# Kernel tuning notes

Measured on AMD Instinct MI355X. Metric: run time of the kernel, lower is better.

Reference implementation:

```python
import jax, jax.numpy as jnp
import numpy as np

B, N, DIM = 4, 2048, 3
H = 128          # hidden
K = 32           # num_neighbours
L = 4            # num_layers
OUT = 6          # out_per_particle


def _dense_init(key, fan_in, fan_out):
    kw, kb = jax.random.split(key)
    w = jax.random.normal(kw, (fan_in, fan_out), jnp.float32) / np.sqrt(fan_in)
    b = jnp.zeros((fan_out,), jnp.float32)
    return w, b


def setup_inputs() -> dict:
    key = jax.random.key(0)
    ks = jax.random.split(key, 8)
    x = jax.random.normal(ks[0], (B, N, DIM), jnp.float32)
    embed_w, embed_b = _dense_init(ks[1], DIM, H)
    # per-layer stacked params
    miw, mib, mow, mob, uiw, uib, uow, uob = [], [], [], [], [], [], [], []
    for l in range(L):
        k0, k1, k2, k3 = jax.random.split(jax.random.fold_in(ks[2], l), 4)
        w, b = _dense_init(k0, 2 * H + 1, H); miw.append(w); mib.append(b)
        w, b = _dense_init(k1, H, H);         mow.append(w); mob.append(b)
        w, b = _dense_init(k2, 2 * H, H);     uiw.append(w); uib.append(b)
        w, b = _dense_init(k3, H, H);         uow.append(w); uob.append(b)
    out_w, out_b = _dense_init(ks[3], H, OUT)
    return {
        'x': x,
        'embed_w': embed_w, 'embed_b': embed_b,
        'msg_in_w': jnp.stack(miw), 'msg_in_b': jnp.stack(mib),
        'msg_out_w': jnp.stack(mow), 'msg_out_b': jnp.stack(mob),
        'upd_in_w': jnp.stack(uiw), 'upd_in_b': jnp.stack(uib),
        'upd_out_w': jnp.stack(uow), 'upd_out_b': jnp.stack(uob),
        'out_w': out_w, 'out_b': out_b,
    }


def reference(x, embed_w, embed_b,
              msg_in_w, msg_in_b, msg_out_w, msg_out_b,
              upd_in_w, upd_in_b, upd_out_w, upd_out_b,
              out_w, out_b):
    act = jax.nn.silu
    n = x.shape[-2]
    # per-particle embed: (B,N,H)
    h = x @ embed_w + embed_b
    # pairwise squared distances (B,N,N), plain Euclidean (geometry=None)
    diff = x[..., :, None, :] - x[..., None, :, :]
    d_sq = jnp.sum(diff * diff, axis=-1)
    eye = jnp.eye(n, dtype=bool)
    d_sq = jnp.where(eye, jnp.inf, d_sq)
    neg_topk, idx_topk = jax.lax.top_k(-d_sq, K)      # (B,N,K)
    d_nearest = jnp.sqrt(jnp.maximum(-neg_topk, 0.0))  # (B,N,K)

    gather = jax.vmap(lambda hb, ib: hb[ib])  # (N,H),(N,K)->(N,K,H) over batch
    n_layers = msg_in_w.shape[0]
    for l in range(n_layers):
        nb = gather(h, idx_topk)                               # (B,N,K,H)
        node_i = jnp.broadcast_to(h[..., :, None, :], nb.shape)
        msg_inp = jnp.concatenate([node_i, nb, d_nearest[..., None]], axis=-1)
        msg = act(msg_inp @ msg_in_w[l] + msg_in_b[l]) @ msg_out_w[l] + msg_out_b[l]
        agg = jnp.sum(msg, axis=-2)                            # (B,N,H)
        upd_inp = jnp.concatenate([h, agg], axis=-1)
        upd = act(upd_inp @ upd_in_w[l] + upd_in_b[l]) @ upd_out_w[l] + upd_out_b[l]
        h = h + upd
    return h @ out_w + out_b
```

## Files before the change

### kernel.cpp

```cpp
#include <hip/hip_runtime.h>
#include <math.h>

#define B_ 4
#define N_ 2048
#define H_ 128
#define K_ 32
#define L_ 4
#define OUT_ 6
#define BN_ (B_*N_)
#define NPB_L 16
#define LBLK 512

typedef __attribute__((ext_vector_type(8))) short short8;
typedef __attribute__((ext_vector_type(4))) float f32x4;

#define LDW (H_ + 8)
#define LAYER_W 98304
#define OFF_W1A 0
#define OFF_W1C 16384
#define OFF_W2  32768
#define OFF_U1  49152
#define OFF_U2  81920
#define SCAP 256
#define KNN_ROWS 4
#define KNN_BLKS (BN_/KNN_ROWS)
#define PREP_BLKS (L_*LAYER_W/256)

__device__ __forceinline__ float silu_f(float x) {
    return __fdividef(x, 1.0f + __expf(-x));
}
__device__ __forceinline__ short f2b(float f) {
    unsigned u = __float_as_uint(f);
    return (short)((u + 0x7FFFu + ((u >> 16) & 1u)) >> 16);
}
__device__ __forceinline__ float b2f(short s) {
    return __uint_as_float(((unsigned)(unsigned short)s) << 16);
}
__device__ __forceinline__ unsigned pack2(short lo, short hi) {
    return (unsigned)(unsigned short)lo | ((unsigned)(unsigned short)hi << 16);
}
__device__ __forceinline__ int mbcnt64(unsigned long long m) {
    return __builtin_amdgcn_mbcnt_hi((unsigned)(m >> 32),
           __builtin_amdgcn_mbcnt_lo((unsigned)m, 0));
}

__global__ __launch_bounds__(256) void k_front(
    const float* __restrict__ x, int* __restrict__ nidx, float* __restrict__ ndist,
    const float* __restrict__ miw, const float* __restrict__ mow,
    const float* __restrict__ uiw, const float* __restrict__ uow,
    short* __restrict__ wt,
    const float* __restrict__ ew, const float* __restrict__ eb,
    const float* __restrict__ mib, float* __restrict__ Epack)
{
    __shared__ float xsx[N_], xsy[N_], xsz[N_];
    __shared__ unsigned skey[KNN_ROWS][SCAP];
    __shared__ int      sid [KNN_ROWS][SCAP];

    if (blockIdx.x >= KNN_BLKS + PREP_BLKS) {
        int t = threadIdx.x;
        int which = t >> 7, n = t & 127;
        const float* W = miw + (size_t)(which ? 128 : 0) * H_;
        float E0 = 0.f, E1 = 0.f, E2 = 0.f, Eb = 0.f;
        for (int k = 0; k < 128; ++k) {
            float w = W[(size_t)k*H_ + n];
            E0 = fmaf(ew[k],       w, E0);
            E1 = fmaf(ew[128 + k], w, E1);
            E2 = fmaf(ew[256 + k], w, E2);
            Eb = fmaf(eb[k],       w, Eb);
        }
        float* dst = Epack + which * 512;
        dst[0*128 + n] = E0;
        dst[1*128 + n] = E1;
        dst[2*128 + n] = E2;
        dst[3*128 + n] = Eb + (which ? 0.f : mib[n]);
        return;
    }
    if (blockIdx.x >= KNN_BLKS) {
        int gid = (blockIdx.x - KNN_BLKS) * 256 + threadIdx.x;
        int l = gid / LAYER_W, o = gid - l * LAYER_W;
        float v;
        if (o < OFF_W1C) {
            int n = o >> 7, k = o & 127;
            v = miw[(size_t)l*257*H_ + k*H_ + n];
        } else if (o < OFF_W2) {
            int oo = o - OFF_W1C, n = oo >> 7, k = oo & 127;
            v = miw[(size_t)l*257*H_ + (128 + k)*H_ + n];
        } else if (o < OFF_U1) {
            int oo = o - OFF_W2, n = oo >> 7, k = oo & 127;
            v = mow[(size_t)l*H_*H_ + k*H_ + n];
        } else if (o < OFF_U2) {
            int oo = o - OFF_U1, n = oo >> 8, k = oo & 255;
            v = uiw[(size_t)l*2*H_*H_ + k*H_ + n];
        } else {
            int oo = o - OFF_U2, n = oo >> 7, k = oo & 127;
            v = uow[(size_t)l*H_*H_ + k*H_ + n];
        }
        wt[gid] = f2b(v);
        return;
    }

    int b  = blockIdx.x / (N_/KNN_ROWS);
    int i0 = (blockIdx.x % (N_/KNN_ROWS)) * KNN_ROWS;
    const float* xb = x + (size_t)b*N_*3;
    for (int t = threadIdx.x; t < N_*3; t += 256) {
        float v = xb[t];
        int q = t / 3, r = t - q*3;
        float* dst = (r == 0) ? xsx : (r == 1) ? xsy : xsz;
        dst[q] = v;
    }
    __syncthreads();

    int wave = threadIdx.x >> 6, lane = threadIdx.x & 63;
    int i = i0 + wave;
    float xix = xsx[i], xiy = xsy[i], xiz = xsz[i];

    unsigned u[N_/64];
    unsigned lmin = 0xFFFFFFFFu;
#pragma unroll
    for (int t = 0; t < N_/64; ++t) {
        int j = lane + 64*t;
        float d0 = xix-xsx[j], d1 = xiy-xsy[j], d2 = xiz-xsz[j];
        float d = d0*d0 + d1*d1 + d2*d2;
        unsigned k = (j == i) ? 0x7F800000u : __float_as_uint(d);
        u[t] = k;
        lmin = min(lmin, k);
    }
    unsigned mn = lmin, mx = lmin;
    for (int off = 32; off; off >>= 1) {
        unsigned o1 = (unsigned)__shfl_xor((int)mn, off); mn = min(mn, o1);
        unsigned o2 = (unsigned)__shfl_xor((int)mx, off); mx = max(mx, o2);
    }
    unsigned Tup = mn;
    if (mn != mx) {
        int hb = 31 - __clz((int)(mn ^ mx));
        Tup = mn & ~((2u << hb) - 1u);
        for (int bit = hb; bit >= 0; --bit) {
            unsigned cand = Tup | (1u << bit);
            if (__popcll(__ballot(lmin < cand)) < K_) Tup = cand;
        }
    }
    unsigned* sk = skey[wave];
    int*      si = sid [wave];
    int base = 0;
#pragma unroll
    for (int t = 0; t < N_/64; ++t) {
        bool pr = (u[t] <= Tup);
        unsigned long long m = __ballot(pr);
        if (pr) {
            int pos = base + mbcnt64(m);
            if (pos < SCAP) { sk[pos] = u[t]; si[pos] = lane + 64*t; }
        }
        base += __popcll(m);
    }
    int c = min(base, SCAP);
    unsigned sv[4]; int iv[4];
#pragma unroll
    for (int q = 0; q < 4; ++q) {
        int slot = lane + 64*q;
        bool ok = slot < c;
        sv[q] = ok ? sk[slot] : 0xFFFFFFFFu;
        iv[q] = ok ? si[slot] : 0;
    }
    unsigned T = mn;
    if (mn != Tup) {
        int hb = 31 - __clz((int)(mn ^ Tup));
        T = mn & ~((2u << hb) - 1u);
        for (int bit = hb; bit >= 0; --bit) {
            unsigned cand = T | (1u << bit);
            int cnt = __popcll(__ballot(sv[0] < cand)) + __popcll(__ballot(sv[1] < cand))
                    + __popcll(__ballot(sv[2] < cand)) + __popcll(__ballot(sv[3] < cand));
            if (cnt < K_) T = cand;
        }
    }
    int cnt_lt = __popcll(__ballot(sv[0] < T)) + __popcll(__ballot(sv[1] < T))
               + __popcll(__ballot(sv[2] < T)) + __popcll(__ballot(sv[3] < T));
    int need = K_ - cnt_lt;
    size_t rbase = ((size_t)(b*N_ + i)) * K_;
    int ltc = 0, eqc = 0;
#pragma unroll
    for (int q = 0; q < 4; ++q) {
        bool lt = sv[q] < T, eq = sv[q] == T;
        unsigned long long mlt = __ballot(lt), meq = __ballot(eq);
        int pp = ltc + mbcnt64(mlt), ee = eqc + mbcnt64(meq);
        ltc += __popcll(mlt); eqc += __popcll(meq);
        int pos = lt ? pp : ((eq && ee < need) ? (cnt_lt + ee) : -1);
        if (pos >= 0) {
            nidx [rbase + pos] = iv[q];
            ndist[rbase + pos] = sqrtf(__uint_as_float(sv[q]));
        }
    }
}

__global__ __launch_bounds__(LBLK, 4) void k_layer0(
    float* __restrict__ h, short* __restrict__ a,
    const int* __restrict__ nidx, const float* __restrict__ ndist,
    const float* __restrict__ wd,
    const short* __restrict__ wl,
    const float* __restrict__ b2, const float* __restrict__ u1b,
    const float* __restrict__ u2b,
    short* __restrict__ c_wr,
    const short* __restrict__ wn, const float* __restrict__ b1n,
    const float* __restrict__ x, const float* __restrict__ ew,
    const float* __restrict__ eb, const float* __restrict__ Epack)
{
    __shared__ __align__(16) short s_l[NPB_L][LDW];
    __shared__ __align__(16) short h_l[NPB_L][LDW];
    __shared__ __align__(16) short agg_l[NPB_L][LDW];
    __shared__ __align__(16) float h32s[NPB_L][H_];
    __shared__ float xjs[NPB_L][K_][3];
    __shared__ float dst_s[NPB_L][K_];
    int blk = blockIdx.x;
    int batch = (blk & 7) >> 1;
    int sub   = ((blk >> 3) << 1) | (blk & 1);
    int node0 = batch * N_ + sub * NPB_L;
    int tid = threadIdx.x;
    int wave = tid >> 6, lane = tid & 63, l15 = lane & 15, quad = lane >> 4;
    int ncol = wave*16 + l15;

    for (int t = tid; t < NPB_L*H_; t += LBLK) {
        int row = t >> 7, ch = t & 127;
        int gr = node0 + row;
        float v = eb[ch];
        v = fmaf(x[gr*3+0], ew[ch], v);
        v = fmaf(x[gr*3+1], ew[H_+ch], v);
        v = fmaf(x[gr*3+2], ew[2*H_+ch], v);
        h_l[row][ch] = f2b(v);
        h32s[row][ch] = v;
    }
    {
        int j = nidx[(size_t)node0*K_ + tid];
        int sm = tid >> 5, sk = tid & 31;
        dst_s[sm][sk] = ndist[(size_t)node0*K_ + tid];
        const float* xp = x + ((size_t)batch*N_ + j)*3;
        xjs[sm][sk][0] = xp[0]; xjs[sm][sk][1] = xp[1]; xjs[sm][sk][2] = xp[2];
    }
    __syncthreads();

    short8 bw2[4], bu1[8], bu2[4];
#pragma unroll
    for (int kk = 0; kk < 4; ++kk)
        bw2[kk] = *(const short8*)(wl + OFF_W2 + (size_t)ncol*H_ + kk*32 + quad*8);
#pragma unroll
    for (int kk = 0; kk < 8; ++kk)
        bu1[kk] = *(const short8*)(wl + OFF_U1 + (size_t)ncol*2*H_ + kk*32 + quad*8);
#pragma unroll
    for (int kk = 0; kk < 4; ++kk)
        bu2[kk] = *(const short8*)(wl + OFF_U2 + (size_t)ncol*H_ + kk*32 + quad*8);

    {
        float wd0 = wd[2*lane], wd1 = wd[2*lane+1];
        int ch0 = 2*lane, ch1 = 2*lane + 1;
        float Ea00 = Epack[ch0],       Ea01 = Epack[ch1];
        float Ea10 = Epack[128+ch0],   Ea11 = Epack[128+ch1];
        float Ea20 = Epack[256+ch0],   Ea21 = Epack[256+ch1];
        float ea0  = Epack[384+ch0],   ea1  = Epack[384+ch1];
        float Ec00 = Epack[512+ch0],   Ec01 = Epack[512+ch1];
        float Ec10 = Epack[640+ch0],   Ec11 = Epack[640+ch1];
        float Ec20 = Epack[768+ch0],   Ec21 = Epack[768+ch1];
        float ec0  = Epack[896+ch0],   ec1  = Epack[896+ch1];
#pragma unroll
        for (int nn = 0; nn < 2; ++nn) {
            int m = wave*2 + nn;
            int gr = node0 + m;
            float xi0 = x[gr*3], xi1 = x[gr*3+1], xi2 = x[gr*3+2];
            float a0 = fmaf(xi2, Ea20, fmaf(xi1, Ea10, fmaf(xi0, Ea00, ea0)));
            float a1 = fmaf(xi2, Ea21, fmaf(xi1, Ea11, fmaf(xi0, Ea01, ea1)));
            float s0 = 0.f, s1 = 0.f;
#pragma unroll
            for (int k = 0; k < K_; ++k) {
                float xj0 = xjs[m][k][0], xj1 = xjs[m][k][1], xj2 = xjs[m][k][2];
                float dd = dst_s[m][k];
                float c0 = fmaf(xj2, Ec20, fmaf(xj1, Ec10, fmaf(xj0, Ec00, ec0)));
                float c1 = fmaf(xj2, Ec21, fmaf(xj1, Ec11, fmaf(xj0, Ec01, ec1)));
                s0 += silu_f(a0 + fmaf(dd, wd0, c0));
                s1 += silu_f(a1 + fmaf(dd, wd1, c1));
            }
            *(unsigned*)&s_l[m][2*lane] = pack2(f2b(s0), f2b(s1));
        }
    }
    __syncthreads();

    f32x4 acc;
    acc = (f32x4){0,0,0,0};
#pragma unroll
    for (int kk = 0; kk < 4; ++kk) {
        int k0 = kk*32 + quad*8;
        short8 af = *(const short8*)&s_l[l15][k0];
        acc = __builtin_amdgcn_mfma_f32_16x16x32_bf16(af, bw2[kk], acc, 0, 0, 0);
    }
    {
        float b2v = b2[ncol] * (float)K_;
#pragma unroll
        for (int r = 0; r < 4; ++r)
            agg_l[quad*4 + r][ncol] = f2b(acc[r] + b2v);
    }
    __syncthreads();

    acc = (f32x4){0,0,0,0};
#pragma unroll
    for (int kk = 0; kk < 8; ++kk) {
        const short (*src)[LDW] = (kk < 4) ? h_l : agg_l;
        int kloc = ((kk < 4) ? kk*32 : (kk-4)*32) + quad*8;
        short8 af = *(const short8*)&src[l15][kloc];
        acc = __builtin_amdgcn_mfma_f32_16x16x32_bf16(af, bu1[kk], acc, 0, 0, 0);
    }
    short8 bacA[4], bacC[4];
#pragma unroll
    for (int kk = 0; kk < 4; ++kk) {
        bacA[kk] = *(const short8*)(wn + OFF_W1A + (size_t)ncol*H_ + kk*32 + quad*8);
        bacC[kk] = *(const short8*)(wn + OFF_W1C + (size_t)ncol*H_ + kk*32 + quad*8);
    }
    {
        float u1bv = u1b[ncol];
#pragma unroll
        for (int r = 0; r < 4; ++r)
            s_l[quad*4 + r][ncol] = f2b(silu_f(acc[r] + u1bv));
    }
    __syncthreads();

    acc = (f32x4){0,0,0,0};
#pragma unroll
    for (int kk = 0; kk < 4; ++kk) {
        int k0 = kk*32 + quad*8;
        short8 af = *(const short8*)&s_l[l15][k0];
        acc = __builtin_amdgcn_mfma_f32_16x16x32_bf16(af, bu2[kk], acc, 0, 0, 0);
    }
    {
        float u2bv = u2b[ncol];
#pragma unroll
        for (int r = 0; r < 4; ++r) {
            int m = quad*4 + r;
            float nh = h32s[m][ncol] + acc[r] + u2bv;
            h[(size_t)(node0+m)*H_ + ncol] = nh;
            h_l[m][ncol] = f2b(nh);
        }
    }
    __syncthreads();
    {
        int n = ncol;
        f32x4 accA = (f32x4){0,0,0,0}, accC = (f32x4){0,0,0,0};
#pragma unroll
        for (int kk = 0; kk < 4; ++kk) {
            int k0 = kk*32 + quad*8;
            short8 af = *(const short8*)&h_l[l15][k0];
            accA = __builtin_amdgcn_mfma_f32_16x16x32_bf16(af, bacA[kk], accA, 0, 0, 0);
            accC = __builtin_amdgcn_mfma_f32_16x16x32_bf16(af, bacC[kk], accC, 0, 0, 0);
        }
        float b1v = b1n[n];
#pragma unroll
        for (int r = 0; r < 4; ++r) {
            int m = quad*4 + r;
            size_t gi = (size_t)(node0+m)*H_ + n;
            a[gi]    = f2b(accA[r] + b1v);
            c_wr[gi] = f2b(accC[r]);
        }
    }
}

__global__ __launch_bounds__(LBLK, 4) void k_layer(
    float* __restrict__ h, short* __restrict__ a,
    const int* __restrict__ nidx, const float* __restrict__ ndist,
    const float* __restrict__ wd,
    const short* __restrict__ wl,
    const float* __restrict__ b2, const float* __restrict__ u1b,
    const float* __restrict__ u2b,
    const short* __restrict__ c_rd, short* __restrict__ c_wr,
    const short* __restrict__ wn, const float* __restrict__ b1n, int do_ac,
    const float* __restrict__ ow, const float* __restrict__ ob,
    float* __restrict__ out)
{
    __shared__ __align__(16) short s_l[NPB_L][LDW];
    __shared__ __align__(16) short h_l[NPB_L][LDW];
    __shared__ __align__(16) short agg_l[NPB_L][LDW];
    __shared__ __align__(16) float h32s[NPB_L][H_];
    __shared__ int   idx_s[NPB_L][K_];
    __shared__ float dst_s[NPB_L][K_];
    int blk = blockIdx.x;
    int batch = (blk & 7) >> 1;
    int sub   = ((blk >> 3) << 1) | (blk & 1);
    int node0 = batch * N_ + sub * NPB_L;
    int tid = threadIdx.x;
    int wave = tid >> 6, lane = tid & 63, l15 = lane & 15, quad = lane >> 4;
    int ncol = wave*16 + l15;

    {
        float4 v = reinterpret_cast<const float4*>(h + (size_t)node0*H_)[tid];
        int row = tid >> 5, col = (tid & 31) * 4;
        h_l[row][col+0] = f2b(v.x); h_l[row][col+1] = f2b(v.y);
        h_l[row][col+2] = f2b(v.z); h_l[row][col+3] = f2b(v.w);
        *(float4*)&h32s[row][col] = v;
    }
    idx_s[tid>>5][tid&31] = nidx[(size_t)node0*K_ + tid];
    dst_s[tid>>5][tid&31] = ndist[(size_t)node0*K_ + tid];
    __syncthreads();

    short8 bw2[4], bu1[8], bu2[4];
#pragma unroll
    for (int kk = 0; kk < 4; ++kk)
        bw2[kk] = *(const short8*)(wl + OFF_W2 + (size_t)ncol*H_ + kk*32 + quad*8);
#pragma unroll
    for (int kk = 0; kk < 8; ++kk)
        bu1[kk] = *(const short8*)(wl + OFF_U1 + (size_t)ncol*2*H_ + kk*32 + quad*8);
#pragma unroll
    for (int kk = 0; kk < 4; ++kk)
        bu2[kk] = *(const short8*)(wl + OFF_U2 + (size_t)ncol*H_ + kk*32 + quad*8);

    {
        float wd0 = wd[2*lane], wd1 = wd[2*lane+1];
        const unsigned* c2 = (const unsigned*)c_rd + (size_t)batch*N_*(H_/2);
        const unsigned* a2 = (const unsigned*)a;
#pragma unroll
        for (int nn = 0; nn < 2; ++nn) {
            int m = wave*2 + nn;
            unsigned av = a2[(size_t)(node0+m)*(H_/2) + lane];
            float a0 = b2f((short)(av & 0xFFFFu)), a1 = b2f((short)(av >> 16));
            unsigned cva[16], cvb[16];
#pragma unroll
            for (int k = 0; k < 16; ++k)
                cva[k] = c2[(size_t)idx_s[m][k]*(H_/2) + lane];
#pragma unroll
            for (int k = 0; k < 16; ++k)
                cvb[k] = c2[(size_t)idx_s[m][16+k]*(H_/2) + lane];
            float s0 = 0.f, s1 = 0.f;
#pragma unroll
            for (int k = 0; k < 16; ++k) {
                float dd = dst_s[m][k];
                s0 += silu_f(a0 + fmaf(dd, wd0, b2f((short)(cva[k] & 0xFFFFu))));
                s1 += silu_f(a1 + fmaf(dd, wd1, b2f((short)(cva[k] >> 16))));
            }
#pragma unroll
            for (int k = 0; k < 16; ++k) {
                float dd = dst_s[m][16+k];
                s0 += silu_f(a0 + fmaf(dd, wd0, b2f((short)(cvb[k] & 0xFFFFu))));
                s1 += silu_f(a1 + fmaf(dd, wd1, b2f((short)(cvb[k] >> 16))));
            }
            *(unsigned*)&s_l[m][2*lane] = pack2(f2b(s0), f2b(s1));
        }
    }
    __syncthreads();

    f32x4 acc;
    acc = (f32x4){0,0,0,0};
#pragma unroll
    for (int kk = 0; kk < 4; ++kk) {
        int k0 = kk*32 + quad*8;
        short8 af = *(const short8*)&s_l[l15][k0];
        acc = __builtin_amdgcn_mfma_f32_16x16x32_bf16(af, bw2[kk], acc, 0, 0, 0);
    }
    {
        float b2v = b2[ncol] * (float)K_;
#pragma unroll
        for (int r = 0; r < 4; ++r)
            agg_l[quad*4 + r][ncol] = f2b(acc[r] + b2v);
    }
    __syncthreads();

    acc = (f32x4){0,0,0,0};
#pragma unroll
    for (int kk = 0; kk < 8; ++kk) {
        const short (*src)[LDW] = (kk < 4) ? h_l : agg_l;
        int kloc = ((kk < 4) ? kk*32 : (kk-4)*32) + quad*8;
        short8 af = *(const short8*)&src[l15][kloc];
        acc = __builtin_amdgcn_mfma_f32_16x16x32_bf16(af, bu1[kk], acc, 0, 0, 0);
    }
    short8 bacA[4], bacC[4];
    if (do_ac) {
#pragma unroll
        for (int kk = 0; kk < 4; ++kk) {
            bacA[kk] = *(const short8*)(wn + OFF_W1A + (size_t)ncol*H_ + kk*32 + quad*8);
            bacC[kk] = *(const short8*)(wn + OFF_W1C + (size_t)ncol*H_ + kk*32 + quad*8);
        }
    }
    {
        float u1bv = u1b[ncol];
#pragma unroll
        for (int r = 0; r < 4; ++r)
            s_l[quad*4 + r][ncol] = f2b(silu_f(acc[r] + u1bv));
    }
    __syncthreads();

    acc = (f32x4){0,0,0,0};
#pragma unroll
    for (int kk = 0; kk < 4; ++kk) {
        int k0 = kk*32 + quad*8;
        short8 af = *(const short8*)&s_l[l15][k0];
        acc = __builtin_amdgcn_mfma_f32_16x16x32_bf16(af, bu2[kk], acc, 0, 0, 0);
    }
    {
        float u2bv = u2b[ncol];
#pragma unroll
        for (int r = 0; r < 4; ++r) {
            int m = quad*4 + r;
            float nh = h32s[m][ncol] + acc[r] + u2bv;
            h[(size_t)(node0+m)*H_ + ncol] = nh;
            if (do_ac) h_l[m][ncol] = f2b(nh);
            else       h32s[m][ncol] = nh;
        }
    }
    if (do_ac) {
        __syncthreads();
        int n = ncol;
        f32x4 accA = (f32x4){0,0,0,0}, accC = (f32x4){0,0,0,0};
#pragma unroll
        for (int kk = 0; kk < 4; ++kk) {
            int k0 = kk*32 + quad*8;
            short8 af = *(const short8*)&h_l[l15][k0];
            accA = __builtin_amdgcn_mfma_f32_16x16x32_bf16(af, bacA[kk], accA, 0, 0, 0);
            accC = __builtin_amdgcn_mfma_f32_16x16x32_bf16(af, bacC[kk], accC, 0, 0, 0);
        }
        float b1v = b1n[n];
#pragma unroll
        for (int r = 0; r < 4; ++r) {
            int m = quad*4 + r;
            size_t gi = (size_t)(node0+m)*H_ + n;
            a[gi]    = f2b(accA[r] + b1v);
            c_wr[gi] = f2b(accC[r]);
        }
    } else {
        __syncthreads();
        if (tid < NPB_L*OUT_) {
            int node = tid / OUT_, o = tid - node*OUT_;
            float accv = ob[o];
            for (int r = 0; r < H_; ++r)
                accv = fmaf(h32s[node][r], ow[r*OUT_ + o], accv);
            out[(size_t)(node0+node)*OUT_ + o] = accv;
        }
    }
}

extern "C" void kernel_launch(void* const* d_in, const int* in_sizes, int n_in,
                              void* d_out, int out_size, void* d_ws, size_t ws_size,
                              hipStream_t stream)
{
    const float* x   = (const float*)d_in[0];
    const float* ew  = (const float*)d_in[1];
    const float* eb  = (const float*)d_in[2];
    const float* miw = (const float*)d_in[3];
    const float* mib = (const float*)d_in[4];
    const float* mow = (const float*)d_in[5];
    const float* mob = (const float*)d_in[6];
    const float* uiw = (const float*)d_in[7];
    const float* uib = (const float*)d_in[8];
    const float* uow = (const float*)d_in[9];
    const float* uob = (const float*)d_in[10];
    const float* ow  = (const float*)d_in[11];
    const float* ob  = (const float*)d_in[12];
    float* out = (float*)d_out;

    char* w = (char*)d_ws;
    float* h  = (float*)w;                         w += (size_t)BN_*H_*4;
    float* nd = (float*)w;                         w += (size_t)BN_*K_*4;
    int*   ni = (int*)w;                           w += (size_t)BN_*K_*4;
    short* a  = (short*)w;                         w += (size_t)BN_*H_*2;
    short* c0 = (short*)w;                         w += (size_t)BN_*H_*2;
    short* c1 = (short*)w;                         w += (size_t)BN_*H_*2;
    short* wt = (short*)w;                         w += (size_t)L_*LAYER_W*2;
    float* Epack = (float*)w;

    k_front<<<KNN_BLKS + PREP_BLKS + 1, 256, 0, stream>>>(x, ni, nd,
        miw, mow, uiw, uow, wt, ew, eb, mib, Epack);
    k_layer0<<<BN_/NPB_L, LBLK, 0, stream>>>(h, a, ni, nd,
        miw + 256*H_, wt,
        mob, uib, uob,
        c1, wt + LAYER_W, mib + H_,
        x, ew, eb, Epack);
    for (int l = 1; l < L_; ++l) {
        const short* c_rd = (l & 1) ? c1 : c0;
        short*       c_wr = (l & 1) ? c0 : c1;
        int do_ac = (l + 1 < L_);
        const short* wn = wt + (size_t)(do_ac ? (l+1) : l) * LAYER_W;
        const float* b1n = mib + (size_t)(do_ac ? (l+1) : l) * H_;
        k_layer<<<BN_/NPB_L, LBLK, 0, stream>>>(h, a, ni, nd,
            miw + (size_t)l*257*H_ + 256*H_,
            wt + (size_t)l*LAYER_W,
            mob + (size_t)l*H_, uib + (size_t)l*H_, uob + (size_t)l*H_,
            c_rd, c_wr, wn, b1n, do_ac,
            ow, ob, out);
    }
}
```

Measured before the change: 225.6 us.

## Fuse layers 1-3 into one persistent kernel with software grid barriers

Replaces the three per-layer k_layer launches with a single k_layers launch. Each block loops over layers 1-3, keeping its node state h in shared memory in fp32, and synchronises the whole grid with an atomic-counter barrier after writing the neighbour projections each layer. The barrier counters are zeroed in k_front. This removes two kernel launch boundaries and the per-layer global writes of h. The atomic barrier adds its own cost and relies on all 512 blocks being co-resident without a cooperative launch, which can deadlock if they are not.

```diff
diff --git a/kernel.cpp b/kernel.cpp
--- a/kernel.cpp
+++ b/kernel.cpp
@@ -25,6 +25,7 @@
 #define KNN_ROWS 4
 #define KNN_BLKS (BN_/KNN_ROWS)
 #define PREP_BLKS (L_*LAYER_W/256)
+#define LAYER_BLKS (BN_/NPB_L)
 
 __device__ __forceinline__ float silu_f(float x) {
     return __fdividef(x, 1.0f + __expf(-x));
@@ -42,6 +43,18 @@
 __device__ __forceinline__ int mbcnt64(unsigned long long m) {
     return __builtin_amdgcn_mbcnt_hi((unsigned)(m >> 32),
            __builtin_amdgcn_mbcnt_lo((unsigned)m, 0));
+}
+
+__device__ __forceinline__ void grid_bar(unsigned* bar, unsigned nblk) {
+    __syncthreads();
+    if (threadIdx.x == 0) {
+        __threadfence();
+        atomicAdd(bar, 1u);
+        while (__hip_atomic_load(bar, __ATOMIC_RELAXED, __HIP_MEMORY_SCOPE_AGENT) < nblk)
+            __builtin_amdgcn_s_sleep(2);
+        __threadfence();
+    }
+    __syncthreads();
 }
 
 __global__ __launch_bounds__(256) void k_front(
@@ -50,7 +63,8 @@
     const float* __restrict__ uiw, const float* __restrict__ uow,
     short* __restrict__ wt,
     const float* __restrict__ ew, const float* __restrict__ eb,
-    const float* __restrict__ mib, float* __restrict__ Epack)
+    const float* __restrict__ mib, float* __restrict__ Epack,
+    unsigned* __restrict__ gbar)
 {
     __shared__ float xsx[N_], xsy[N_], xsz[N_];
     __shared__ unsigned skey[KNN_ROWS][SCAP];
@@ -58,6 +72,7 @@
 
     if (blockIdx.x >= KNN_BLKS + PREP_BLKS) {
         int t = threadIdx.x;
+        if (t < 2) gbar[t] = 0u;
         int which = t >> 7, n = t & 127;
         const float* W = miw + (size_t)(which ? 128 : 0) * H_;
         float E0 = 0.f, E1 = 0.f, E2 = 0.f, Eb = 0.f;
@@ -357,17 +372,15 @@
     }
 }
 
-__global__ __launch_bounds__(LBLK, 4) void k_layer(
-    float* __restrict__ h, short* __restrict__ a,
+__global__ __launch_bounds__(LBLK, 4) void k_layers(
+    const float* __restrict__ h, short* __restrict__ a,
     const int* __restrict__ nidx, const float* __restrict__ ndist,
-    const float* __restrict__ wd,
-    const short* __restrict__ wl,
-    const float* __restrict__ b2, const float* __restrict__ u1b,
-    const float* __restrict__ u2b,
-    const short* __restrict__ c_rd, short* __restrict__ c_wr,
-    const short* __restrict__ wn, const float* __restrict__ b1n, int do_ac,
+    const float* __restrict__ miw, const short* __restrict__ wt,
+    const float* __restrict__ mob, const float* __restrict__ uib,
+    const float* __restrict__ uob, const float* __restrict__ mib,
+    short* __restrict__ c0buf, short* __restrict__ c1buf,
     const float* __restrict__ ow, const float* __restrict__ ob,
-    float* __restrict__ out)
+    float* __restrict__ out, unsigned* __restrict__ gbar)
 {
     __shared__ __align__(16) short s_l[NPB_L][LDW];
     __shared__ __align__(16) short h_l[NPB_L][LDW];
@@ -394,137 +407,150 @@
     dst_s[tid>>5][tid&31] = ndist[(size_t)node0*K_ + tid];
     __syncthreads();
 
-    short8 bw2[4], bu1[8], bu2[4];
-#pragma unroll
-    for (int kk = 0; kk < 4; ++kk)
-        bw2[kk] = *(const short8*)(wl + OFF_W2 + (size_t)ncol*H_ + kk*32 + quad*8);
-#pragma unroll
-    for (int kk = 0; kk < 8; ++kk)
-        bu1[kk] = *(const short8*)(wl + OFF_U1 + (size_t)ncol*2*H_ + kk*32 + quad*8);
-#pragma unroll
-    for (int kk = 0; kk < 4; ++kk)
-        bu2[kk] = *(const short8*)(wl + OFF_U2 + (size_t)ncol*H_ + kk*32 + quad*8);
-
-    {
-        float wd0 = wd[2*lane], wd1 = wd[2*lane+1];
-        const unsigned* c2 = (const unsigned*)c_rd + (size_t)batch*N_*(H_/2);
-        const unsigned* a2 = (const unsigned*)a;
-#pragma unroll
-        for (int nn = 0; nn < 2; ++nn) {
-            int m = wave*2 + nn;
-            unsigned av = a2[(size_t)(node0+m)*(H_/2) + lane];
-            float a0 = b2f((short)(av & 0xFFFFu)), a1 = b2f((short)(av >> 16));
-            unsigned cva[16], cvb[16];
-#pragma unroll
-            for (int k = 0; k < 16; ++k)
-                cva[k] = c2[(size_t)idx_s[m][k]*(H_/2) + lane];
-#pragma unroll
-            for (int k = 0; k < 16; ++k)
-                cvb[k] = c2[(size_t)idx_s[m][16+k]*(H_/2) + lane];
-            float s0 = 0.f, s1 = 0.f;
-#pragma unroll
-            for (int k = 0; k < 16; ++k) {
-                float dd = dst_s[m][k];
-                s0 += silu_f(a0 + fmaf(dd, wd0, b2f((short)(cva[k] & 0xFFFFu))));
-                s1 += silu_f(a1 + fmaf(dd, wd1, b2f((short)(cva[k] >> 16))));
+    for (int l = 1; l < L_; ++l) {
+        int do_ac = (l + 1 < L_);
+        const short* wl  = wt  + (size_t)l * LAYER_W;
+        const float* wd  = miw + (size_t)l*257*H_ + 256*H_;
+        const short* c_rd = (l & 1) ? c1buf : c0buf;
+        short*       c_wr = (l & 1) ? c0buf : c1buf;
+        const float* b2  = mob + (size_t)l*H_;
+        const float* u1b = uib + (size_t)l*H_;
+        const float* u2b = uob + (size_t)l*H_;
+        const short* wn  = wt  + (size_t)(do_ac ? (l+1) : l) * LAYER_W;
+        const float* b1n = mib + (size_t)(do_ac ? (l+1) : l) * H_;
+
+        short8 bw2[4], bu1[8], bu2[4];
+#pragma unroll
+        for (int kk = 0; kk < 4; ++kk)
+            bw2[kk] = *(const short8*)(wl + OFF_W2 + (size_t)ncol*H_ + kk*32 + quad*8);
+#pragma unroll
+        for (int kk = 0; kk < 8; ++kk)
+            bu1[kk] = *(const short8*)(wl + OFF_U1 + (size_t)ncol*2*H_ + kk*32 + quad*8);
+#pragma unroll
+        for (int kk = 0; kk < 4; ++kk)
+            bu2[kk] = *(const short8*)(wl + OFF_U2 + (size_t)ncol*H_ + kk*32 + quad*8);
+
+        {
+            float wd0 = wd[2*lane], wd1 = wd[2*lane+1];
+            const unsigned* c2 = (const unsigned*)c_rd + (size_t)batch*N_*(H_/2);
+            const unsigned* a2 = (const unsigned*)a;
+#pragma unroll
+            for (int nn = 0; nn < 2; ++nn) {
+                int m = wave*2 + nn;
+                unsigned av = a2[(size_t)(node0+m)*(H_/2) + lane];
+                float a0 = b2f((short)(av & 0xFFFFu)), a1 = b2f((short)(av >> 16));
+                unsigned cva[16], cvb[16];
+#pragma unroll
+                for (int k = 0; k < 16; ++k)
+                    cva[k] = c2[(size_t)idx_s[m][k]*(H_/2) + lane];
+#pragma unroll
+                for (int k = 0; k < 16; ++k)
+                    cvb[k] = c2[(size_t)idx_s[m][16+k]*(H_/2) + lane];
+                float s0 = 0.f, s1 = 0.f;
+#pragma unroll
+                for (int k = 0; k < 16; ++k) {
+                    float dd = dst_s[m][k];
+                    s0 += silu_f(a0 + fmaf(dd, wd0, b2f((short)(cva[k] & 0xFFFFu))));
+                    s1 += silu_f(a1 + fmaf(dd, wd1, b2f((short)(cva[k] >> 16))));
+                }
+#pragma unroll
+                for (int k = 0; k < 16; ++k) {
+                    float dd = dst_s[m][16+k];
+                    s0 += silu_f(a0 + fmaf(dd, wd0, b2f((short)(cvb[k] & 0xFFFFu))));
+                    s1 += silu_f(a1 + fmaf(dd, wd1, b2f((short)(cvb[k] >> 16))));
+                }
+                *(unsigned*)&s_l[m][2*lane] = pack2(f2b(s0), f2b(s1));
             }
-#pragma unroll
-            for (int k = 0; k < 16; ++k) {
-                float dd = dst_s[m][16+k];
-                s0 += silu_f(a0 + fmaf(dd, wd0, b2f((short)(cvb[k] & 0xFFFFu))));
-                s1 += silu_f(a1 + fmaf(dd, wd1, b2f((short)(cvb[k] >> 16))));
-            }
-            *(unsigned*)&s_l[m][2*lane] = pack2(f2b(s0), f2b(s1));
-        }
-    }
-    __syncthreads();
-
-    f32x4 acc;
-    acc = (f32x4){0,0,0,0};
-#pragma unroll
-    for (int kk = 0; kk < 4; ++kk) {
-        int k0 = kk*32 + quad*8;
-        short8 af = *(const short8*)&s_l[l15][k0];
-        acc = __builtin_amdgcn_mfma_f32_16x16x32_bf16(af, bw2[kk], acc, 0, 0, 0);
-    }
-    {
-        float b2v = b2[ncol] * (float)K_;
-#pragma unroll
-        for (int r = 0; r < 4; ++r)
-            agg_l[quad*4 + r][ncol] = f2b(acc[r] + b2v);
-    }
-    __syncthreads();
-
-    acc = (f32x4){0,0,0,0};
-#pragma unroll
-    for (int kk = 0; kk < 8; ++kk) {
-        const short (*src)[LDW] = (kk < 4) ? h_l : agg_l;
-        int kloc = ((kk < 4) ? kk*32 : (kk-4)*32) + quad*8;
-        short8 af = *(const short8*)&src[l15][kloc];
-        acc = __builtin_amdgcn_mfma_f32_16x16x32_bf16(af, bu1[kk], acc, 0, 0, 0);
-    }
-    short8 bacA[4], bacC[4];
-    if (do_ac) {
-#pragma unroll
-        for (int kk = 0; kk < 4; ++kk) {
-            bacA[kk] = *(const short8*)(wn + OFF_W1A + (size_t)ncol*H_ + kk*32 + quad*8);
-            bacC[kk] = *(const short8*)(wn + OFF_W1C + (size_t)ncol*H_ + kk*32 + quad*8);
-        }
-    }
-    {
-        float u1bv = u1b[ncol];
-#pragma unroll
-        for (int r = 0; r < 4; ++r)
-            s_l[quad*4 + r][ncol] = f2b(silu_f(acc[r] + u1bv));
-    }
-    __syncthreads();
-
-    acc = (f32x4){0,0,0,0};
-#pragma unroll
-    for (int kk = 0; kk < 4; ++kk) {
-        int k0 = kk*32 + quad*8;
-        short8 af = *(const short8*)&s_l[l15][k0];
-        acc = __builtin_amdgcn_mfma_f32_16x16x32_bf16(af, bu2[kk], acc, 0, 0, 0);
-    }
-    {
-        float u2bv = u2b[ncol];
-#pragma unroll
-        for (int r = 0; r < 4; ++r) {
-            int m = quad*4 + r;
-            float nh = h32s[m][ncol] + acc[r] + u2bv;
-            h[(size_t)(node0+m)*H_ + ncol] = nh;
-            if (do_ac) h_l[m][ncol] = f2b(nh);
-            else       h32s[m][ncol] = nh;
-        }
-    }
-    if (do_ac) {
+        }
         __syncthreads();
-        int n = ncol;
-        f32x4 accA = (f32x4){0,0,0,0}, accC = (f32x4){0,0,0,0};
+
+        f32x4 acc;
+        acc = (f32x4){0,0,0,0};
 #pragma unroll
         for (int kk = 0; kk < 4; ++kk) {
             int k0 = kk*32 + quad*8;
-            short8 af = *(const short8*)&h_l[l15][k0];
-            accA = __builtin_amdgcn_mfma_f32_16x16x32_bf16(af, bacA[kk], accA, 0, 0, 0);
-            accC = __builtin_amdgcn_mfma_f32_16x16x32_bf16(af, bacC[kk], accC, 0, 0, 0);
-        }
-        float b1v = b1n[n];
-#pragma unroll
-        for (int r = 0; r < 4; ++r) {
-            int m = quad*4 + r;
-            size_t gi = (size_t)(node0+m)*H_ + n;
-            a[gi]    = f2b(accA[r] + b1v);
-            c_wr[gi] = f2b(accC[r]);
-        }
-    } else {
+            short8 af = *(const short8*)&s_l[l15][k0];
+            acc = __builtin_amdgcn_mfma_f32_16x16x32_bf16(af, bw2[kk], acc, 0, 0, 0);
+        }
+        {
+            float b2v = b2[ncol] * (float)K_;
+#pragma unroll
+            for (int r = 0; r < 4; ++r)
+                agg_l[quad*4 + r][ncol] = f2b(acc[r] + b2v);
+        }
         __syncthreads();
-        if (tid < NPB_L*OUT_) {
-            int node = tid / OUT_, o = tid - node*OUT_;
-            float accv = ob[o];
-            for (int r = 0; r < H_; ++r)
-                accv = fmaf(h32s[node][r], ow[r*OUT_ + o], accv);
-            out[(size_t)(node0+node)*OUT_ + o] = accv;
-        }
+
+        acc = (f32x4){0,0,0,0};
+#pragma unroll
+        for (int kk = 0; kk < 8; ++kk) {
+            const short (*src)[LDW] = (kk < 4) ? h_l : agg_l;
+            int kloc = ((kk < 4) ? kk*32 : (kk-4)*32) + quad*8;
+            short8 af = *(const short8*)&src[l15][kloc];
+            acc = __builtin_amdgcn_mfma_f32_16x16x32_bf16(af, bu1[kk], acc, 0, 0, 0);
+        }
+        short8 bacA[4], bacC[4];
+        if (do_ac) {
+#pragma unroll
+            for (int kk = 0; kk < 4; ++kk) {
+                bacA[kk] = *(const short8*)(wn + OFF_W1A + (size_t)ncol*H_ + kk*32 + quad*8);
+                bacC[kk] = *(const short8*)(wn + OFF_W1C + (size_t)ncol*H_ + kk*32 + quad*8);
+            }
+        }
+        {
+            float u1bv = u1b[ncol];
+#pragma unroll
+            for (int r = 0; r < 4; ++r)
+                s_l[quad*4 + r][ncol] = f2b(silu_f(acc[r] + u1bv));
+        }
+        __syncthreads();
+
+        acc = (f32x4){0,0,0,0};
+#pragma unroll
+        for (int kk = 0; kk < 4; ++kk) {
+            int k0 = kk*32 + quad*8;
+            short8 af = *(const short8*)&s_l[l15][k0];
+            acc = __builtin_amdgcn_mfma_f32_16x16x32_bf16(af, bu2[kk], acc, 0, 0, 0);
+        }
+        {
+            float u2bv = u2b[ncol];
+#pragma unroll
+            for (int r = 0; r < 4; ++r) {
+                int m = quad*4 + r;
+                float nh = h32s[m][ncol] + acc[r] + u2bv;
+                h32s[m][ncol] = nh;
+                if (do_ac) h_l[m][ncol] = f2b(nh);
+            }
+        }
+        if (do_ac) {
+            __syncthreads();
+            int n = ncol;
+            f32x4 accA = (f32x4){0,0,0,0}, accC = (f32x4){0,0,0,0};
+#pragma unroll
+            for (int kk = 0; kk < 4; ++kk) {
+                int k0 = kk*32 + quad*8;
+                short8 af = *(const short8*)&h_l[l15][k0];
+                accA = __builtin_amdgcn_mfma_f32_16x16x32_bf16(af, bacA[kk], accA, 0, 0, 0);
+                accC = __builtin_amdgcn_mfma_f32_16x16x32_bf16(af, bacC[kk], accC, 0, 0, 0);
+            }
+            float b1v = b1n[n];
+#pragma unroll
+            for (int r = 0; r < 4; ++r) {
+                int m = quad*4 + r;
+                size_t gi = (size_t)(node0+m)*H_ + n;
+                a[gi]    = f2b(accA[r] + b1v);
+                c_wr[gi] = f2b(accC[r]);
+            }
+            grid_bar(gbar + (l - 1), LAYER_BLKS);
+        }
+    }
+
+    __syncthreads();
+    if (tid < NPB_L*OUT_) {
+        int node = tid / OUT_, o = tid - node*OUT_;
+        float accv = ob[o];
+        for (int r = 0; r < H_; ++r)
+            accv = fmaf(h32s[node][r], ow[r*OUT_ + o], accv);
+        out[(size_t)(node0+node)*OUT_ + o] = accv;
     }
 }
 
@@ -555,26 +581,17 @@
     short* c0 = (short*)w;                         w += (size_t)BN_*H_*2;
     short* c1 = (short*)w;                         w += (size_t)BN_*H_*2;
     short* wt = (short*)w;                         w += (size_t)L_*LAYER_W*2;
-    float* Epack = (float*)w;
+    float* Epack = (float*)w;                      w += (size_t)1024*4;
+    unsigned* gbar = (unsigned*)w;
 
     k_front<<<KNN_BLKS + PREP_BLKS + 1, 256, 0, stream>>>(x, ni, nd,
-        miw, mow, uiw, uow, wt, ew, eb, mib, Epack);
+        miw, mow, uiw, uow, wt, ew, eb, mib, Epack, gbar);
     k_layer0<<<BN_/NPB_L, LBLK, 0, stream>>>(h, a, ni, nd,
         miw + 256*H_, wt,
         mob, uib, uob,
         c1, wt + LAYER_W, mib + H_,
         x, ew, eb, Epack);
-    for (int l = 1; l < L_; ++l) {
-        const short* c_rd = (l & 1) ? c1 : c0;
-        short*       c_wr = (l & 1) ? c0 : c1;
-        int do_ac = (l + 1 < L_);
-        const short* wn = wt + (size_t)(do_ac ? (l+1) : l) * LAYER_W;
-        const float* b1n = mib + (size_t)(do_ac ? (l+1) : l) * H_;
-        k_layer<<<BN_/NPB_L, LBLK, 0, stream>>>(h, a, ni, nd,
-            miw + (size_t)l*257*H_ + 256*H_,
-            wt + (size_t)l*LAYER_W,
-            mob + (size_t)l*H_, uib + (size_t)l*H_, uob + (size_t)l*H_,
-            c_rd, c_wr, wn, b1n, do_ac,
-            ow, ob, out);
-    }
-}
+    k_layers<<<LAYER_BLKS, LBLK, 0, stream>>>(h, a, ni, nd,
+        miw, wt, mob, uib, uob, mib,
+        c0, c1, ow, ob, out, gbar);
+}
```

Result: slower. 338.2 us (+49.9%).
